# Performance work log

Measured on AMD Instinct MI355X. Metric: run time of the kernel, lower is better.

The kernel has to match this reference:

```python
import jax, jax.numpy as jnp
import numpy as np

B, T, C, H = 8, 1024, 768, 12
HD = C // H  # 64, even for RoPE
ROPE_THETA = 10000.0


def precompute_freqs_cis(dim, end, theta=ROPE_THETA):
    # [end, dim//2, 2] with (cos, sin) in last axis
    freqs = 1.0 / theta ** (jnp.arange(0, dim // 2).astype(jnp.float32) / (dim // 2))
    t = jnp.arange(end)
    f = jnp.outer(t, freqs)
    return jnp.stack([jnp.cos(f), jnp.sin(f)], axis=-1)


def apply_rope(x, fc):
    # x: [B,T,H,hd]; fc: [T,1,hd//2,2] (broadcasts over B and H)
    xr = x.reshape(*x.shape[:-1], -1, 2)
    x_re, x_im = xr[..., 0], xr[..., 1]
    cos, sin = fc[..., 0], fc[..., 1]
    out_re = x_re * cos - x_im * sin
    out_im = x_re * sin + x_im * cos
    return jnp.stack([out_re, out_im], axis=-1).reshape(x.shape)


def setup_inputs() -> dict:
    key = jax.random.key(0)
    k0, k1, k2 = jax.random.split(key, 3)
    x = jax.random.normal(k0, (B, T, C), jnp.float32)
    Wqkv = jax.random.normal(k1, (C, 3 * C), jnp.float32) * 0.02
    bqkv = jnp.zeros((3 * C,), jnp.float32)
    Wproj = jax.random.normal(k2, (C, C), jnp.float32) * 0.02
    bproj = jnp.zeros((C,), jnp.float32)
    mask = jnp.tril(jnp.ones((T, T), jnp.int32))  # causal
    return {"x": x, "Wqkv": Wqkv, "bqkv": bqkv, "Wproj": Wproj, "bproj": bproj, "mask": mask}


def reference(x, Wqkv, bqkv, Wproj, bproj, mask):
    B_, T_, C_ = x.shape
    qkv = (x @ Wqkv + bqkv).reshape(B_, T_, 3, H, HD)
    q, k, v = qkv[:, :, 0], qkv[:, :, 1], qkv[:, :, 2]  # each [B,T,H,hd]
    fc = precompute_freqs_cis(HD, T_)[:, None]  # [T,1,hd//2,2]
    q = apply_rope(q, fc)
    k = apply_rope(k, fc)
    scale = 1.0 / jnp.sqrt(jnp.float32(HD))
    attn = jnp.einsum('bthd,bkhd->bhtk', q, k) * scale  # [B,H,T,T]
    neg = jnp.finfo(attn.dtype).min
    attn = jnp.where(mask[None, None, :, :] == 0, neg, attn)
    attn = jax.nn.softmax(attn, axis=-1)
    out = jnp.einsum('bhtk,bkhd->bthd', attn, v).reshape(B_, T_, C_)
    return out @ Wproj + bproj
```

## Files before the change

kernel.cpp:

```cpp
#include <hip/hip_runtime.h>
#include <cstdint>
#include <cstddef>

#define BB 8
#define TT 1024
#define CC 768
#define NH 12
#define HD 64

using bf16x8 = __attribute__((ext_vector_type(8))) short;
using f32x4  = __attribute__((ext_vector_type(4))) float;

static __device__ __forceinline__ short f2bf(float f) {
    uint32_t u;
    __builtin_memcpy(&u, &f, 4);
    u += 0x7FFFu + ((u >> 16) & 1u);
    return (short)(u >> 16);
}

static __device__ __forceinline__ uint32_t bfpack(float lo, float hi) {
    return (uint32_t)(uint16_t)f2bf(lo) | ((uint32_t)(uint16_t)f2bf(hi) << 16);
}

#define GLOAD_LDS16(gp, lp)                                                        \
    __builtin_amdgcn_global_load_lds(                                              \
        (const __attribute__((address_space(1))) void*)(gp),                       \
        (__attribute__((address_space(3))) void*)(lp), 16, 0, 0)

__global__ void fc_kernel(float2* __restrict__ fc) {
    int idx = blockIdx.x * 256 + threadIdx.x;
    int t = idx >> 5, p = idx & 31;
    float freq = powf(10000.0f, -(float)p / 32.0f);
    float a = (float)t * freq;
    fc[idx] = make_float2(cosf(a), sinf(a));
}

__global__ __launch_bounds__(256)
void cast_kernel(const float* __restrict__ in, short* __restrict__ out) {
    int i = (blockIdx.x * 256 + threadIdx.x) * 8;
    float4 f0 = *(const float4*)(in + i);
    float4 f1 = *(const float4*)(in + i + 4);
    bf16x8 h;
    h[0] = f2bf(f0.x); h[1] = f2bf(f0.y); h[2] = f2bf(f0.z); h[3] = f2bf(f0.w);
    h[4] = f2bf(f1.x); h[5] = f2bf(f1.y); h[6] = f2bf(f1.z); h[7] = f2bf(f1.w);
    *(bf16x8*)(out + i) = h;
}

__global__ __launch_bounds__(256)
void transpose_cast_kernel(const float* __restrict__ in, short* __restrict__ out,
                           int R, int Cdim) {
    __shared__ float tile[32][33];
    int tx = threadIdx.x, ty = threadIdx.y;
    int c0 = blockIdx.x * 32, r0 = blockIdx.y * 32;
#pragma unroll
    for (int i = 0; i < 4; i++)
        tile[ty + 8 * i][tx] = in[(size_t)(r0 + ty + 8 * i) * Cdim + c0 + tx];
    __syncthreads();
#pragma unroll
    for (int i = 0; i < 4; i++)
        out[(size_t)(c0 + ty + 8 * i) * R + r0 + tx] = f2bf(tile[tx][ty + 8 * i]);
}

__global__ __launch_bounds__(256)
void vtrans_kernel(const short* __restrict__ V, short* __restrict__ VT) {
    __shared__ short tl[64][72];
    const int tid = threadIdx.x;
    const int bh = blockIdx.y, t0 = blockIdx.x * 64;
    {
        int r = tid >> 2, cs = (tid & 3) * 16;
        const short* src = V + (size_t)bh * TT * HD + (size_t)(t0 + r) * HD + cs;
        *(bf16x8*)&tl[r][cs]     = *(const bf16x8*)src;
        *(bf16x8*)&tl[r][cs + 8] = *(const bf16x8*)(src + 8);
    }
    __syncthreads();
    {
        int d = tid >> 2, ts = (tid & 3) * 16;
        bf16x8 o0, o1;
#pragma unroll
        for (int e = 0; e < 8; e++) { o0[e] = tl[ts + e][d]; o1[e] = tl[ts + 8 + e][d]; }
        short* dst = VT + (size_t)bh * TT * HD + (size_t)d * TT + t0 + ts;
        *(bf16x8*)dst       = o0;
        *(bf16x8*)(dst + 8) = o1;
    }
}

template <int EPI>
__global__ __launch_bounds__(256)
void gemm_kernel(const short* __restrict__ Agl, const short* __restrict__ BT,
                 const float* __restrict__ bias,
                 short* __restrict__ Qb, short* __restrict__ Kb, short* __restrict__ Vb,
                 const float2* __restrict__ fc, float* __restrict__ out) {
    __shared__ __align__(16) char smem[32768];
    short* As = (short*)smem;
    short* Bs = (short*)(smem + 16384);
    const int tid = threadIdx.x;
    const int lane = tid & 63, wid = tid >> 6;
    const int g = lane >> 4, c = lane & 15;
    const int wm = wid >> 1, wn = wid & 1;

    const int bid = blockIdx.y * gridDim.x + blockIdx.x;
    const int cpx = (gridDim.x * gridDim.y) >> 3;
    const int swz = (bid & 7) * cpx + (bid >> 3);
    const int m0 = (swz / gridDim.x) * 128, n0 = (swz % gridDim.x) * 128;

    const f32x4 zero4 = {0.f, 0.f, 0.f, 0.f};
    f32x4 acc[4][4];
#pragma unroll
    for (int i = 0; i < 4; i++)
#pragma unroll
        for (int j = 0; j < 4; j++) acc[i][j] = zero4;

    const int rowb = lane >> 3;
    const int colb = (lane & 7) * 8;

    for (int k0 = 0; k0 < 768; k0 += 64) {
        const short* ga = Agl + (size_t)(m0 + wid * 32 + rowb) * 768 + k0 + colb;
        const short* gb = BT  + (size_t)(n0 + wid * 32 + rowb) * 768 + k0 + colb;
#pragma unroll
        for (int q = 0; q < 4; q++) {
            GLOAD_LDS16(ga + (size_t)q * 8 * 768, As + (wid * 32 + q * 8) * 64);
            GLOAD_LDS16(gb + (size_t)q * 8 * 768, Bs + (wid * 32 + q * 8) * 64);
        }
        __syncthreads();
#pragma unroll
        for (int kk = 0; kk < 2; kk++) {
            bf16x8 af[4], bfr[4];
#pragma unroll
            for (int mi = 0; mi < 4; mi++)
                af[mi] = *(const bf16x8*)&As[(wm * 64 + mi * 16 + c) * 64 + kk * 32 + g * 8];
#pragma unroll
            for (int ni = 0; ni < 4; ni++)
                bfr[ni] = *(const bf16x8*)&Bs[(wn * 64 + ni * 16 + c) * 64 + kk * 32 + g * 8];
#pragma unroll
            for (int mi = 0; mi < 4; mi++)
#pragma unroll
                for (int ni = 0; ni < 4; ni++)
                    acc[mi][ni] = __builtin_amdgcn_mfma_f32_16x16x32_bf16(
                        af[mi], bfr[ni], acc[mi][ni], 0, 0, 0);
        }
        __syncthreads();
    }

    if (EPI == 0) {
        uint32_t* LD = (uint32_t*)smem;
#pragma unroll
        for (int ni = 0; ni < 4; ni++) {
            int nl = wn * 64 + ni * 16 + c;
            int n = n0 + nl;
            float bv = bias[n];
            int part = (n >= 1536) ? 2 : (n >= 768 ? 1 : 0);
            int d = (n - part * 768) & 63;
#pragma unroll
            for (int mi = 0; mi < 4; mi++) {
#pragma unroll
                for (int r = 0; r < 4; r++) {
                    int ml = wm * 64 + mi * 16 + g * 4 + r;
                    float v = acc[mi][ni][r] + bv;
                    float pv = __shfl_xor(v, 1);
                    if (!(c & 1)) {
                        float o0, o1;
                        if (part < 2) {
                            int t = (m0 + ml) & 1023;
                            float2 cs = fc[t * 32 + (d >> 1)];
                            o0 = v * cs.x - pv * cs.y;
                            o1 = v * cs.y + pv * cs.x;
                            if (part == 0) { o0 *= 0.125f; o1 *= 0.125f; }
                        } else { o0 = v; o1 = pv; }
                        LD[ml * 64 + ((nl >> 1) ^ (((ml >> 2) & 3) << 3))] = bfpack(o0, o1);
                    }
                }
            }
        }
        __syncthreads();
#pragma unroll
        for (int p = 0; p < 8; p++) {
            int ml = p * 16 + (tid >> 4);
            int wc = (tid & 15) * 4;
            int4 dat = *(const int4*)&LD[ml * 64 + (wc ^ (((ml >> 2) & 3) << 3))];
            int n = n0 + wc * 2;
            int part = (n >= 1536) ? 2 : (n >= 768 ? 1 : 0);
            int rem = n - part * 768;
            int h = rem >> 6, d = rem & 63;
            int m = m0 + ml, b = m >> 10, t = m & 1023;
            short* dst = (part == 0 ? Qb : part == 1 ? Kb : Vb)
                         + (((size_t)b * NH + h) * TT + t) * HD + d;
            *(int4*)dst = dat;
        }
    } else {
#pragma unroll
        for (int mi = 0; mi < 4; mi++)
#pragma unroll
            for (int ni = 0; ni < 4; ni++) {
                int n = n0 + wn * 64 + ni * 16 + c;
                float bv = bias[n];
#pragma unroll
                for (int r = 0; r < 4; r++) {
                    int m = m0 + wm * 64 + mi * 16 + g * 4 + r;
                    out[(size_t)m * CC + n] = acc[mi][ni][r] + bv;
                }
            }
    }
}

__global__ __launch_bounds__(256)
void attn_kernel(const short* __restrict__ Qb, const short* __restrict__ Kb,
                 const short* __restrict__ VT, short* __restrict__ Ob) {
    __shared__ uint32_t Pt[4][32][32];
    __shared__ uint32_t ot[128 * 32];
    const int tid = threadIdx.x, lane = tid & 63, wid = tid >> 6;
    const int g = lane >> 4, c = lane & 15;
    const int bh = blockIdx.x, qb = 7 - (int)blockIdx.y;
    const int b = bh / NH, h = bh % NH;
    const short* Qp = Qb + (size_t)bh * TT * HD;
    const short* Kp = Kb + (size_t)bh * TT * HD;
    const short* Vp = VT + (size_t)bh * TT * HD;
    const int q0 = qb * 128 + wid * 32;
    const int sw = (c & 7) << 2;

    bf16x8 qf[2][2];
#pragma unroll
    for (int qs = 0; qs < 2; qs++)
#pragma unroll
        for (int kh = 0; kh < 2; kh++)
            qf[qs][kh] = *(const bf16x8*)(Qp + (size_t)(q0 + qs * 16 + c) * HD + kh * 32 + g * 8);

    const f32x4 zero4 = {0.f, 0.f, 0.f, 0.f};
    f32x4 o[2][4];
#pragma unroll
    for (int qs = 0; qs < 2; qs++)
#pragma unroll
        for (int dt = 0; dt < 4; dt++) o[qs][dt] = zero4;
    float mrun[2] = {-1e30f, -1e30f}, lrun[2] = {0.f, 0.f};

    const int t0max = ((q0 + 31) >> 6) << 6;
    for (int t0 = 0; t0 <= t0max; t0 += 64) {
        f32x4 st[2][4];
#pragma unroll
        for (int nt = 0; nt < 4; nt++) {
            const short* kp = Kp + (size_t)(t0 + nt * 16 + c) * HD + g * 8;
            bf16x8 k0 = *(const bf16x8*)kp;
            bf16x8 k1 = *(const bf16x8*)(kp + 32);
#pragma unroll
            for (int qs = 0; qs < 2; qs++) {
                f32x4 z = zero4;
                z = __builtin_amdgcn_mfma_f32_16x16x32_bf16(k0, qf[qs][0], z, 0, 0, 0);
                z = __builtin_amdgcn_mfma_f32_16x16x32_bf16(k1, qf[qs][1], z, 0, 0, 0);
                st[qs][nt] = z;
            }
        }
        bf16x8 vf[2][4];
#pragma unroll
        for (int blk = 0; blk < 2; blk++)
#pragma unroll
            for (int dt = 0; dt < 4; dt++)
                vf[blk][dt] = *(const bf16x8*)(Vp + (size_t)(dt * 16 + c) * TT + t0 + blk * 32 + g * 8);
        if (t0 + 63 > q0) {
#pragma unroll
            for (int qs = 0; qs < 2; qs++) {
                int q = q0 + qs * 16 + c;
#pragma unroll
                for (int nt = 0; nt < 4; nt++)
#pragma unroll
                    for (int r = 0; r < 4; r++)
                        if (t0 + nt * 16 + g * 4 + r > q) st[qs][nt][r] = -1e30f;
            }
        }
#pragma unroll
        for (int qs = 0; qs < 2; qs++) {
            float mx = st[qs][0][0];
#pragma unroll
            for (int nt = 0; nt < 4; nt++)
#pragma unroll
                for (int r = 0; r < 4; r++) mx = fmaxf(mx, st[qs][nt][r]);
            mx = fmaxf(mx, __shfl_xor(mx, 16));
            mx = fmaxf(mx, __shfl_xor(mx, 32));
            float mnew = fmaxf(mrun[qs], mx);
            float al = __expf(mrun[qs] - mnew);
            mrun[qs] = mnew;
            float sm = 0.f;
#pragma unroll
            for (int nt = 0; nt < 4; nt++)
#pragma unroll
                for (int r = 0; r < 4; r++) {
                    float e = __expf(st[qs][nt][r] - mnew);
                    st[qs][nt][r] = e;
                    sm += e;
                }
            sm += __shfl_xor(sm, 16);
            sm += __shfl_xor(sm, 32);
            lrun[qs] = lrun[qs] * al + sm;
#pragma unroll
            for (int dt = 0; dt < 4; dt++) {
                o[qs][dt][0] *= al; o[qs][dt][1] *= al;
                o[qs][dt][2] *= al; o[qs][dt][3] *= al;
            }
            int row = qs * 16 + c;
#pragma unroll
            for (int nt = 0; nt < 4; nt++) {
                uint32_t w0 = bfpack(st[qs][nt][0], st[qs][nt][1]);
                uint32_t w1 = bfpack(st[qs][nt][2], st[qs][nt][3]);
                int wa = nt * 8 + 2 * g;
                Pt[wid][row][wa ^ sw]       = w0;
                Pt[wid][row][(wa + 1) ^ sw] = w1;
            }
        }
#pragma unroll
        for (int qs = 0; qs < 2; qs++) {
            int row = qs * 16 + c;
#pragma unroll
            for (int blk = 0; blk < 2; blk++) {
                bf16x8 pf = *(const bf16x8*)&Pt[wid][row][(blk * 16 + 4 * g) ^ sw];
#pragma unroll
                for (int dt = 0; dt < 4; dt++)
                    o[qs][dt] = __builtin_amdgcn_mfma_f32_16x16x32_bf16(
                        vf[blk][dt], pf, o[qs][dt], 0, 0, 0);
            }
        }
    }

#pragma unroll
    for (int qs = 0; qs < 2; qs++) {
        float inv = 1.0f / lrun[qs];
        int ql = wid * 32 + qs * 16 + c;
#pragma unroll
        for (int dt = 0; dt < 4; dt++) {
            uint32_t w0 = bfpack(o[qs][dt][0] * inv, o[qs][dt][1] * inv);
            uint32_t w1 = bfpack(o[qs][dt][2] * inv, o[qs][dt][3] * inv);
            int jc0 = dt * 8 + 2 * g;
            int jc1 = jc0 + 1;
            ot[ql * 32 + ((((jc0 >> 2) ^ (c & 7)) << 2) | (jc0 & 3))] = w0;
            ot[ql * 32 + ((((jc1 >> 2) ^ (c & 7)) << 2) | (jc1 & 3))] = w1;
        }
    }
    __syncthreads();
#pragma unroll
    for (int p = 0; p < 4; p++) {
        int q = (tid >> 3) + 32 * p;
        int jb = tid & 7;
        const uint32_t* src = &ot[q * 32 + ((jb ^ (q & 7)) << 2)];
        int4 w = *(const int4*)src;
        *(int4*)(Ob + ((size_t)b * TT + qb * 128 + q) * CC + h * HD + jb * 8) = w;
    }
}

extern "C" void kernel_launch(void* const* d_in, const int* in_sizes, int n_in,
                              void* d_out, int out_size, void* d_ws, size_t ws_size,
                              hipStream_t stream) {
    const float* x     = (const float*)d_in[0];
    const float* Wqkv  = (const float*)d_in[1];
    const float* bqkv  = (const float*)d_in[2];
    const float* Wproj = (const float*)d_in[3];
    const float* bproj = (const float*)d_in[4];

    char* ws = (char*)d_ws;
    short*  WqkvT  = (short*)(ws);
    short*  WprojT = (short*)(ws + 3538944);
    float2* fc     = (float2*)(ws + 3538944 + 1179648);
    short*  Qb     = (short*)(ws + 4980736);
    short*  Kb     = (short*)(ws + 4980736 + 1 * 12582912);
    short*  VOb    = (short*)(ws + 4980736 + 2 * 12582912);
    short*  VbT    = (short*)(ws + 4980736 + 3 * 12582912);
    short*  xb     = VbT;
    float*  out    = (float*)d_out;

    hipLaunchKernelGGL(fc_kernel, dim3(128), dim3(256), 0, stream, fc);
    hipLaunchKernelGGL(transpose_cast_kernel, dim3(72, 24), dim3(32, 8), 0, stream,
                       Wqkv, WqkvT, 768, 2304);
    hipLaunchKernelGGL(transpose_cast_kernel, dim3(24, 24), dim3(32, 8), 0, stream,
                       Wproj, WprojT, 768, 768);
    hipLaunchKernelGGL(cast_kernel, dim3(3072), dim3(256), 0, stream, x, xb);
    hipLaunchKernelGGL((gemm_kernel<0>), dim3(18, 64), dim3(256), 0, stream,
                       xb, WqkvT, bqkv, Qb, Kb, VOb, fc, (float*)nullptr);
    hipLaunchKernelGGL(vtrans_kernel, dim3(16, 96), dim3(256), 0, stream, VOb, VbT);
    hipLaunchKernelGGL(attn_kernel, dim3(96, 8), dim3(256), 0, stream, Qb, Kb, VbT, VOb);
    hipLaunchKernelGGL((gemm_kernel<1>), dim3(6, 64), dim3(256), 0, stream,
                       VOb, WprojT, bproj,
                       (short*)nullptr, (short*)nullptr, (short*)nullptr,
                       (const float2*)nullptr, out);
}
```

Baseline: 192.3 us.

## Double-buffer GEMM with 128x256 tiles, 512 threads and swizzled LDS layout

```diff
diff --git a/kernel.cpp b/kernel.cpp
--- a/kernel.cpp
+++ b/kernel.cpp
@@ -85,23 +85,40 @@
 }
 
 template <int EPI>
-__global__ __launch_bounds__(256)
+__global__ __launch_bounds__(512)
 void gemm_kernel(const short* __restrict__ Agl, const short* __restrict__ BT,
                  const float* __restrict__ bias,
                  short* __restrict__ Qb, short* __restrict__ Kb, short* __restrict__ Vb,
                  const float2* __restrict__ fc, float* __restrict__ out) {
-    __shared__ __align__(16) char smem[32768];
-    short* As = (short*)smem;
-    short* Bs = (short*)(smem + 16384);
+    __shared__ __align__(16) char smem[98304];
     const int tid = threadIdx.x;
     const int lane = tid & 63, wid = tid >> 6;
     const int g = lane >> 4, c = lane & 15;
-    const int wm = wid >> 1, wn = wid & 1;
-
-    const int bid = blockIdx.y * gridDim.x + blockIdx.x;
-    const int cpx = (gridDim.x * gridDim.y) >> 3;
+    const int wm = wid >> 2, wn = wid & 3;
+
+    const int nx = gridDim.x;
+    const int bid = blockIdx.y * nx + blockIdx.x;
+    const int cpx = (nx * gridDim.y) >> 3;
     const int swz = (bid & 7) * cpx + (bid >> 3);
-    const int m0 = (swz / gridDim.x) * 128, n0 = (swz % gridDim.x) * 128;
+    const int m0 = (swz / nx) * 128, n0 = (swz % nx) * 256;
+
+    const int srow = tid >> 2;
+    const int sblk = tid & 3;
+    const int scol0 = ((sblk ^ ((srow >> 1) & 3)) << 3);
+
+    const short* Abase = Agl + (size_t)(m0 + srow) * 768 + scol0;
+    const short* Bbase0 = BT + (size_t)(n0 + srow) * 768 + scol0;
+    const short* Bbase1 = BT + (size_t)(n0 + 128 + srow) * 768 + scol0;
+
+#define A_SLOT(b, kh) (smem + (b) * 49152 + (kh) * 8192 + wid * 1024)
+#define B_SLOT(b, kh, q) (smem + (b) * 49152 + 16384 + (kh) * 16384 + (q) * 8192 + wid * 1024)
+#define STAGE(b, kh, kt)                                                   \
+    {                                                                      \
+        int koff = (kt) * 64 + (kh) * 32;                                  \
+        GLOAD_LDS16(Abase + koff, A_SLOT(b, kh));                          \
+        GLOAD_LDS16(Bbase0 + koff, B_SLOT(b, kh, 0));                      \
+        GLOAD_LDS16(Bbase1 + koff, B_SLOT(b, kh, 1));                      \
+    }
 
     const f32x4 zero4 = {0.f, 0.f, 0.f, 0.f};
     f32x4 acc[4][4];
@@ -110,38 +127,50 @@
 #pragma unroll
         for (int j = 0; j < 4; j++) acc[i][j] = zero4;
 
-    const int rowb = lane >> 3;
-    const int colb = (lane & 7) * 8;
-
-    for (int k0 = 0; k0 < 768; k0 += 64) {
-        const short* ga = Agl + (size_t)(m0 + wid * 32 + rowb) * 768 + k0 + colb;
-        const short* gb = BT  + (size_t)(n0 + wid * 32 + rowb) * 768 + k0 + colb;
-#pragma unroll
-        for (int q = 0; q < 4; q++) {
-            GLOAD_LDS16(ga + (size_t)q * 8 * 768, As + (wid * 32 + q * 8) * 64);
-            GLOAD_LDS16(gb + (size_t)q * 8 * 768, Bs + (wid * 32 + q * 8) * 64);
-        }
-        __syncthreads();
+    STAGE(0, 0, 0);
+    STAGE(0, 1, 0);
+    STAGE(1, 0, 1);
+    asm volatile("s_waitcnt vmcnt(6)" ::: "memory");
+    __builtin_amdgcn_s_barrier();
+
+    for (int t = 0; t < 12; t++) {
+        const int buf = t & 1;
+        const int t1 = (t + 1 < 12) ? t + 1 : t - 11;
+        const int t2 = (t + 2 < 12) ? t + 2 : t - 10;
 #pragma unroll
         for (int kk = 0; kk < 2; kk++) {
+            const short* Ab = (const short*)(smem + buf * 49152 + kk * 8192);
+            const short* Bb = (const short*)(smem + buf * 49152 + 16384 + kk * 16384);
             bf16x8 af[4], bfr[4];
 #pragma unroll
-            for (int mi = 0; mi < 4; mi++)
-                af[mi] = *(const bf16x8*)&As[(wm * 64 + mi * 16 + c) * 64 + kk * 32 + g * 8];
-#pragma unroll
-            for (int ni = 0; ni < 4; ni++)
-                bfr[ni] = *(const bf16x8*)&Bs[(wn * 64 + ni * 16 + c) * 64 + kk * 32 + g * 8];
+            for (int mi = 0; mi < 4; mi++) {
+                int row = wm * 64 + mi * 16 + c;
+                af[mi] = *(const bf16x8*)&Ab[row * 32 + ((g ^ ((row >> 1) & 3)) << 3)];
+            }
+#pragma unroll
+            for (int ni = 0; ni < 4; ni++) {
+                int row = wn * 64 + ni * 16 + c;
+                bfr[ni] = *(const bf16x8*)&Bb[row * 32 + ((g ^ ((row >> 1) & 3)) << 3)];
+            }
+            if (kk == 0) STAGE(buf ^ 1, 1, t1)
+            else         STAGE(buf, 0, t2)
+            __builtin_amdgcn_s_barrier();
+            __builtin_amdgcn_s_setprio(1);
 #pragma unroll
             for (int mi = 0; mi < 4; mi++)
 #pragma unroll
                 for (int ni = 0; ni < 4; ni++)
                     acc[mi][ni] = __builtin_amdgcn_mfma_f32_16x16x32_bf16(
                         af[mi], bfr[ni], acc[mi][ni], 0, 0, 0);
-        }
-        __syncthreads();
+            __builtin_amdgcn_s_setprio(0);
+            asm volatile("s_waitcnt vmcnt(6)" ::: "memory");
+            __builtin_amdgcn_s_barrier();
+        }
     }
 
     if (EPI == 0) {
+        asm volatile("s_waitcnt vmcnt(0)" ::: "memory");
+        __builtin_amdgcn_s_barrier();
         uint32_t* LD = (uint32_t*)smem;
 #pragma unroll
         for (int ni = 0; ni < 4; ni++) {
@@ -166,7 +195,7 @@
                             o1 = v * cs.y + pv * cs.x;
                             if (part == 0) { o0 *= 0.125f; o1 *= 0.125f; }
                         } else { o0 = v; o1 = pv; }
-                        LD[ml * 64 + ((nl >> 1) ^ (((ml >> 2) & 3) << 3))] = bfpack(o0, o1);
+                        LD[ml * 128 + ((nl >> 1) ^ (((ml >> 2) & 3) << 3))] = bfpack(o0, o1);
                     }
                 }
             }
@@ -174,10 +203,10 @@
         __syncthreads();
 #pragma unroll
         for (int p = 0; p < 8; p++) {
-            int ml = p * 16 + (tid >> 4);
-            int wc = (tid & 15) * 4;
-            int4 dat = *(const int4*)&LD[ml * 64 + (wc ^ (((ml >> 2) & 3) << 3))];
-            int n = n0 + wc * 2;
+            int ml = p * 16 + (tid >> 5);
+            int wg = tid & 31;
+            int4 dat = *(const int4*)&LD[ml * 128 + ((wg * 4) ^ (((ml >> 2) & 3) << 3))];
+            int n = n0 + wg * 8;
             int part = (n >= 1536) ? 2 : (n >= 768 ? 1 : 0);
             int rem = n - part * 768;
             int h = rem >> 6, d = rem & 63;
@@ -200,6 +229,9 @@
                 }
             }
     }
+#undef A_SLOT
+#undef B_SLOT
+#undef STAGE
 }
 
 __global__ __launch_bounds__(256)
@@ -369,11 +401,11 @@
     hipLaunchKernelGGL(transpose_cast_kernel, dim3(24, 24), dim3(32, 8), 0, stream,
                        Wproj, WprojT, 768, 768);
     hipLaunchKernelGGL(cast_kernel, dim3(3072), dim3(256), 0, stream, x, xb);
-    hipLaunchKernelGGL((gemm_kernel<0>), dim3(18, 64), dim3(256), 0, stream,
+    hipLaunchKernelGGL((gemm_kernel<0>), dim3(9, 64), dim3(512), 0, stream,
                        xb, WqkvT, bqkv, Qb, Kb, VOb, fc, (float*)nullptr);
     hipLaunchKernelGGL(vtrans_kernel, dim3(16, 96), dim3(256), 0, stream, VOb, VbT);
     hipLaunchKernelGGL(attn_kernel, dim3(96, 8), dim3(256), 0, stream, Qb, Kb, VbT, VOb);
-    hipLaunchKernelGGL((gemm_kernel<1>), dim3(6, 64), dim3(256), 0, stream,
+    hipLaunchKernelGGL((gemm_kernel<1>), dim3(3, 64), dim3(512), 0, stream,
                        VOb, WprojT, bproj,
                        (short*)nullptr, (short*)nullptr, (short*)nullptr,
                        (const float2*)nullptr, out);
```

After: 173.5 us. 9.8% less time.

## Double-buffer GEMM through registers with XOR-swizzled LDS and MFMA priority

Applied to the files above, without the earlier changes.

```diff
diff --git a/kernel.cpp b/kernel.cpp
--- a/kernel.cpp
+++ b/kernel.cpp
@@ -21,11 +21,6 @@
 static __device__ __forceinline__ uint32_t bfpack(float lo, float hi) {
     return (uint32_t)(uint16_t)f2bf(lo) | ((uint32_t)(uint16_t)f2bf(hi) << 16);
 }
-
-#define GLOAD_LDS16(gp, lp)                                                        \
-    __builtin_amdgcn_global_load_lds(                                              \
-        (const __attribute__((address_space(1))) void*)(gp),                       \
-        (__attribute__((address_space(3))) void*)(lp), 16, 0, 0)
 
 __global__ void fc_kernel(float2* __restrict__ fc) {
     int idx = blockIdx.x * 256 + threadIdx.x;
@@ -85,23 +80,28 @@
 }
 
 template <int EPI>
-__global__ __launch_bounds__(256)
+__global__ __launch_bounds__(256, 2)
 void gemm_kernel(const short* __restrict__ Agl, const short* __restrict__ BT,
                  const float* __restrict__ bias,
                  short* __restrict__ Qb, short* __restrict__ Kb, short* __restrict__ Vb,
                  const float2* __restrict__ fc, float* __restrict__ out) {
-    __shared__ __align__(16) char smem[32768];
-    short* As = (short*)smem;
-    short* Bs = (short*)(smem + 16384);
+    __shared__ __align__(16) short As[2][128 * 64];
+    __shared__ __align__(16) short Bs[2][128 * 64];
     const int tid = threadIdx.x;
     const int lane = tid & 63, wid = tid >> 6;
     const int g = lane >> 4, c = lane & 15;
     const int wm = wid >> 1, wn = wid & 1;
 
-    const int bid = blockIdx.y * gridDim.x + blockIdx.x;
-    const int cpx = (gridDim.x * gridDim.y) >> 3;
+    const int nx = gridDim.x;
+    const int bid = blockIdx.y * nx + blockIdx.x;
+    const int cpx = (nx * gridDim.y) >> 3;
     const int swz = (bid & 7) * cpx + (bid >> 3);
-    const int m0 = (swz / gridDim.x) * 128, n0 = (swz % gridDim.x) * 128;
+    const int m0 = (swz / nx) * 128, n0 = (swz % nx) * 128;
+
+    const int srow = lane >> 2;
+    const int sch = lane & 3;
+    const short* Ab0 = Agl + (size_t)(m0 + wid * 32 + srow) * 768 + sch * 8;
+    const short* Bb0 = BT  + (size_t)(n0 + wid * 32 + srow) * 768 + sch * 8;
 
     const f32x4 zero4 = {0.f, 0.f, 0.f, 0.f};
     f32x4 acc[4][4];
@@ -110,39 +110,82 @@
 #pragma unroll
         for (int j = 0; j < 4; j++) acc[i][j] = zero4;
 
-    const int rowb = lane >> 3;
-    const int colb = (lane & 7) * 8;
-
-    for (int k0 = 0; k0 < 768; k0 += 64) {
-        const short* ga = Agl + (size_t)(m0 + wid * 32 + rowb) * 768 + k0 + colb;
-        const short* gb = BT  + (size_t)(n0 + wid * 32 + rowb) * 768 + k0 + colb;
-#pragma unroll
-        for (int q = 0; q < 4; q++) {
-            GLOAD_LDS16(ga + (size_t)q * 8 * 768, As + (wid * 32 + q * 8) * 64);
-            GLOAD_LDS16(gb + (size_t)q * 8 * 768, Bs + (wid * 32 + q * 8) * 64);
-        }
+    bf16x8 rA[4], rB[4];
+#define LOAD(kt)                                                               \
+    {                                                                          \
+        size_t ko = (size_t)(kt) * 64;                                         \
+        _Pragma("unroll")                                                      \
+        for (int q = 0; q < 2; q++)                                            \
+            _Pragma("unroll")                                                  \
+            for (int h = 0; h < 2; h++) {                                      \
+                rA[q * 2 + h] = *(const bf16x8*)(Ab0 + (size_t)q * 16 * 768 + ko + h * 32); \
+                rB[q * 2 + h] = *(const bf16x8*)(Bb0 + (size_t)q * 16 * 768 + ko + h * 32); \
+            }                                                                  \
+    }
+#define WRITE(buf)                                                             \
+    {                                                                          \
+        _Pragma("unroll")                                                      \
+        for (int q = 0; q < 2; q++)                                            \
+            _Pragma("unroll")                                                  \
+            for (int h = 0; h < 2; h++) {                                      \
+                int row = wid * 32 + q * 16 + srow;                            \
+                int ci = sch + h * 4;                                          \
+                int idx = row * 64 + ((ci ^ (row & 7)) * 8);                   \
+                *(bf16x8*)&As[buf][idx] = rA[q * 2 + h];                       \
+                *(bf16x8*)&Bs[buf][idx] = rB[q * 2 + h];                       \
+            }                                                                  \
+    }
+#define COMPUTE(buf)                                                           \
+    {                                                                          \
+        _Pragma("unroll")                                                      \
+        for (int kk = 0; kk < 2; kk++) {                                       \
+            bf16x8 af[4], bfr[4];                                              \
+            _Pragma("unroll")                                                  \
+            for (int mi = 0; mi < 4; mi++) {                                   \
+                int row = wm * 64 + mi * 16 + c;                               \
+                af[mi] = *(const bf16x8*)&As[buf][row * 64 + (((kk * 4 + g) ^ (row & 7)) * 8)]; \
+            }                                                                  \
+            _Pragma("unroll")                                                  \
+            for (int ni = 0; ni < 4; ni++) {                                   \
+                int row = wn * 64 + ni * 16 + c;                               \
+                bfr[ni] = *(const bf16x8*)&Bs[buf][row * 64 + (((kk * 4 + g) ^ (row & 7)) * 8)]; \
+            }                                                                  \
+            __builtin_amdgcn_s_setprio(1);                                     \
+            _Pragma("unroll")                                                  \
+            for (int mi = 0; mi < 4; mi++)                                     \
+                _Pragma("unroll")                                              \
+                for (int ni = 0; ni < 4; ni++)                                 \
+                    acc[mi][ni] = __builtin_amdgcn_mfma_f32_16x16x32_bf16(     \
+                        af[mi], bfr[ni], acc[mi][ni], 0, 0, 0);                \
+            __builtin_amdgcn_s_setprio(0);                                     \
+        }                                                                      \
+    }
+
+    LOAD(0);
+    WRITE(0);
+    __syncthreads();
+
+#pragma unroll 1
+    for (int t2 = 0; t2 < 12; t2 += 2) {
+        LOAD(t2 + 1);
+        COMPUTE(0);
         __syncthreads();
-#pragma unroll
-        for (int kk = 0; kk < 2; kk++) {
-            bf16x8 af[4], bfr[4];
-#pragma unroll
-            for (int mi = 0; mi < 4; mi++)
-                af[mi] = *(const bf16x8*)&As[(wm * 64 + mi * 16 + c) * 64 + kk * 32 + g * 8];
-#pragma unroll
-            for (int ni = 0; ni < 4; ni++)
-                bfr[ni] = *(const bf16x8*)&Bs[(wn * 64 + ni * 16 + c) * 64 + kk * 32 + g * 8];
-#pragma unroll
-            for (int mi = 0; mi < 4; mi++)
-#pragma unroll
-                for (int ni = 0; ni < 4; ni++)
-                    acc[mi][ni] = __builtin_amdgcn_mfma_f32_16x16x32_bf16(
-                        af[mi], bfr[ni], acc[mi][ni], 0, 0, 0);
-        }
+        WRITE(1);
         __syncthreads();
+        if (t2 + 2 < 12) {
+            LOAD(t2 + 2);
+            COMPUTE(1);
+            __syncthreads();
+            WRITE(0);
+            __syncthreads();
+        } else {
+            COMPUTE(1);
+        }
     }
 
     if (EPI == 0) {
-        uint32_t* LD = (uint32_t*)smem;
+        __syncthreads();
+        uint32_t* LD = (uint32_t*)&As[0][0];
 #pragma unroll
         for (int ni = 0; ni < 4; ni++) {
             int nl = wn * 64 + ni * 16 + c;
@@ -200,6 +243,9 @@
                 }
             }
     }
+#undef LOAD
+#undef WRITE
+#undef COMPUTE
 }
 
 __global__ __launch_bounds__(256)
```

After: 173.2 us. -10.0%, faster.
